# Kernel tuning notes

Measured on AMD Instinct MI355X. Metric: run time of the kernel, lower is better.

The kernel has to match this reference:

```python
import jax, jax.numpy as jnp
import numpy as np


def _gather_nbrs(atoms, edges):
    # atoms [B,N,F], edges [B,N,D] (neighbor indices) -> [B,N,D,F]
    return jax.vmap(lambda a, e: a[e])(atoms, edges)


def _linear(x, W, b):
    return x @ W + b


def setup_inputs() -> dict:
    key = jax.random.key(0)
    ks = jax.random.split(key, 32)
    B, Nm, Dm, Fa, Fb = 64, 64, 6, 37, 6      # molecules
    Np, Dp, Fp = 512, 12, 480                  # proteins
    HM, HP, NC = 128, 128, 1

    def rn(k, shape):
        return jax.random.normal(k, shape, jnp.float32) * 0.05

    return {
        'm_atoms': jax.random.normal(ks[0], (B, Nm, Fa), jnp.float32),
        'm_bonds': jax.random.normal(ks[1], (B, Nm, Dm, Fb), jnp.float32),
        'm_edges': jax.random.randint(ks[2], (B, Nm, Dm), 0, Nm, jnp.int32),
        'p_atoms': jax.random.normal(ks[3], (B, Np, Fp), jnp.float32),
        'p_edges': jax.random.randint(ks[4], (B, Np, Dp), 0, Np, jnp.int32),
        # GraphConv mol 1: in 43 = 37 atom + 6 bond
        'W1': rn(ks[5], (43, 128)), 'b1': jnp.zeros((128,), jnp.float32),
        # GraphConv mol 2: in 134 = 128 + 6
        'W2': rn(ks[6], (134, 128)), 'b2': jnp.zeros((128,), jnp.float32),
        # GraphConv_p 1/2
        'Wp1': rn(ks[7], (480, 200)), 'bp1': jnp.zeros((200,), jnp.float32),
        'Wp2': rn(ks[8], (200, 100)), 'bp2': jnp.zeros((100,), jnp.float32),
        # GraphOutput (134 -> hid_dim_m), GraphOutput_p (100 -> hid_dim_p)
        'Wo': rn(ks[9], (134, HM)), 'bo': jnp.zeros((HM,), jnp.float32),
        'Wop': rn(ks[10], (100, HP)), 'bop': jnp.zeros((HP,), jnp.float32),
        # FC stack
        'Wf1': rn(ks[11], (HM + HP, 100)), 'bf1': jnp.zeros((100,), jnp.float32),
        'Wf2': rn(ks[12], (100, 100)), 'bf2': jnp.zeros((100,), jnp.float32),
        'Wout': rn(ks[13], (100, NC)), 'bout': jnp.zeros((NC,), jnp.float32),
    }


def reference(m_atoms, m_bonds, m_edges, p_atoms, p_edges,
              W1, b1, W2, b2, Wp1, bp1, Wp2, bp2,
              Wo, bo, Wop, bop, Wf1, bf1, Wf2, bf2, Wout, bout):
    def gconv_mol(atoms, W, b):
        # self + summed-neighbor atom features, concat summed bond features
        nbr_sum = _gather_nbrs(atoms, m_edges).sum(2)           # [B,N,F]
        summed = jnp.concatenate([atoms + nbr_sum, m_bonds.sum(2)], axis=-1)
        return _linear(summed, W, b)

    def gconv_pro(atoms, W, b):
        nbr_sum = _gather_nbrs(atoms, p_edges).sum(2)
        return _linear(atoms + nbr_sum, W, b)

    a = jax.nn.relu(gconv_mol(m_atoms, W1, b1))
    a = jax.nn.relu(gconv_mol(a, W2, b2))
    # GraphOutput: tanh(linear(cat[atoms, bond_sum])) summed over atoms
    fp_m = jnp.tanh(_linear(jnp.concatenate([a, m_bonds.sum(2)], -1), Wo, bo)).sum(1)

    p = jax.nn.relu(gconv_pro(p_atoms, Wp1, bp1))
    p = jax.nn.relu(gconv_pro(p, Wp2, bp2))
    fp_p = jnp.tanh(_linear(p, Wop, bop)).sum(1)

    fp = jnp.concatenate([fp_m, fp_p], axis=1)
    # NOTE: source applies FC1 then FC2 with no activation in between
    fp = _linear(_linear(fp, Wf1, bf1), Wf2, bf2)
    return jax.nn.sigmoid(_linear(fp, Wout, bout))
```

## Files before the change

### kernel.cpp

```cpp
#include <hip/hip_runtime.h>
#include <cmath>

#define B   64
#define NM  64
#define DM  6
#define FA  37
#define FB  6
#define NP  512
#define DP  12
#define FPD 480
#define HM  128
#define HP  128

typedef _Float16 half8 __attribute__((ext_vector_type(8)));
typedef float f32x4 __attribute__((ext_vector_type(4)));

static const size_t OFF_FPP  = 0;
static const size_t OFF_Z    = OFF_FPP + (size_t)B*128;
static const size_t OFF_P    = OFF_Z   + (size_t)B*NP*200;
static const size_t OFF_W16  = OFF_P   + (size_t)B*NP*200 + 256;
#define W16_WT1   0
#define W16_WT2   107520
#define W16_WTOP  132608
#define W16_MW1T  148992
#define W16_MW2T  157184
#define W16_MWOT  177664
#define W16_TOT   198144

__device__ __forceinline__ float4 f4add(float4 a, float4 b) {
    return make_float4(a.x + b.x, a.y + b.y, a.z + b.z, a.w + b.w);
}

__device__ __forceinline__ half8 load_a_frag(const float* p) {
    float4 f0 = *(const float4*)(p);
    float4 f1 = *(const float4*)(p + 4);
    half8 h;
    h[0] = (_Float16)f0.x; h[1] = (_Float16)f0.y; h[2] = (_Float16)f0.z; h[3] = (_Float16)f0.w;
    h[4] = (_Float16)f1.x; h[5] = (_Float16)f1.y; h[6] = (_Float16)f1.z; h[7] = (_Float16)f1.w;
    return h;
}

__global__ void k_prep(const float* __restrict__ Wp1, const float* __restrict__ Wp2,
                       const float* __restrict__ Wop,
                       const float* __restrict__ W1,  const float* __restrict__ W2,
                       const float* __restrict__ Wo,  _Float16* __restrict__ w16) {
    int idx = blockIdx.x * 256 + threadIdx.x;
    if (idx < 224 * 480) {
        int n = idx / 480, k = idx % 480;
        w16[idx] = (n < 200) ? (_Float16)Wp1[k * 200 + n] : (_Float16)0.f;
    } else if (idx < W16_WTOP) {
        int r = idx - W16_WT2;
        int n = r / 224, k = r % 224;
        w16[idx] = (n < 100 && k < 200) ? (_Float16)Wp2[k * 100 + n] : (_Float16)0.f;
    } else if (idx < W16_MW1T) {
        int r = idx - W16_WTOP;
        int n = r >> 7, k = r & 127;
        w16[idx] = (k < 100) ? (_Float16)Wop[k * 128 + n] : (_Float16)0.f;
    } else if (idx < W16_MW2T) {
        int r = idx - W16_MW1T;
        int n = r >> 6, k = r & 63;
        w16[idx] = (k < 43) ? (_Float16)W1[k * 128 + n] : (_Float16)0.f;
    } else if (idx < W16_MWOT) {
        int r = idx - W16_MW2T;
        int n = r / 160, k = r % 160;
        w16[idx] = (k < 134) ? (_Float16)W2[k * 128 + n] : (_Float16)0.f;
    } else if (idx < W16_TOT) {
        int r = idx - W16_MWOT;
        int n = r / 160, k = r % 160;
        w16[idx] = (k < 134) ? (_Float16)Wo[k * 128 + n] : (_Float16)0.f;
    }
}

__global__ __launch_bounds__(256) void k_zp1(
        const float* __restrict__ A, const _Float16* __restrict__ Wt,
        float* __restrict__ Z) {
    int tid = threadIdx.x, lane = tid & 63, wid = tid >> 6;
    int rw = wid & 1, cw = wid >> 1;
    int rbase = blockIdx.x * 64 + rw * 32;
    int cbase = cw * 112;
    int lr = lane & 15, lk = (lane >> 4) * 8;
    f32x4 acc[2][7] = {};
    const float* Ar0 = A + (size_t)(rbase + lr) * FPD + lk;
    const float* Ar1 = A + (size_t)(rbase + 16 + lr) * FPD + lk;
    for (int k0 = 0; k0 < FPD; k0 += 32) {
        half8 a0 = load_a_frag(Ar0 + k0);
        half8 a1 = load_a_frag(Ar1 + k0);
        #pragma unroll
        for (int nt = 0; nt < 7; ++nt) {
            half8 b = *(const half8*)&Wt[(size_t)(cbase + nt * 16 + lr) * FPD + k0 + lk];
            acc[0][nt] = __builtin_amdgcn_mfma_f32_16x16x32_f16(a0, b, acc[0][nt], 0, 0, 0);
            acc[1][nt] = __builtin_amdgcn_mfma_f32_16x16x32_f16(a1, b, acc[1][nt], 0, 0, 0);
        }
    }
    int rj = (lane >> 4) * 4;
    #pragma unroll
    for (int nt = 0; nt < 7; ++nt) {
        int col = cbase + nt * 16 + lr;
        if (col < 200) {
            #pragma unroll
            for (int mt = 0; mt < 2; ++mt)
                #pragma unroll
                for (int j = 0; j < 4; ++j)
                    Z[(size_t)(rbase + mt * 16 + rj + j) * 200 + col] = acc[mt][nt][j];
        }
    }
}

__global__ __launch_bounds__(256) void k_ga1(
        const float* __restrict__ Z, const int* __restrict__ edges,
        const float* __restrict__ bias, float* __restrict__ out) {
    int bid = blockIdx.x;
    int x = bid & 7, j = bid >> 3;
    int b = (j >> 5) * 8 + x, tile = j & 31;
    int n0 = tile * 16, tid = threadIdx.x;
    __shared__ int e[16 * DP];
    if (tid < 16 * DP)
        e[tid] = edges[(b * NP + n0 + tid / DP) * DP + tid % DP];
    __syncthreads();
    const float4* Zb = (const float4*)(Z + (size_t)b * NP * 200);
    float4* ob = (float4*)(out + (size_t)b * NP * 200);
    const float4* b4 = (const float4*)bias;
    for (int idx = tid; idx < 16 * 50; idx += 256) {
        int r = idx / 50, c = idx % 50;
        float4 v = Zb[(n0 + r) * 50 + c];
        #pragma unroll
        for (int d = 0; d < DP; ++d) v = f4add(v, Zb[e[r * DP + d] * 50 + c]);
        v = f4add(v, b4[c]);
        ob[(n0 + r) * 50 + c] = make_float4(fmaxf(v.x, 0.f), fmaxf(v.y, 0.f),
                                            fmaxf(v.z, 0.f), fmaxf(v.w, 0.f));
    }
}

__global__ __launch_bounds__(256) void k_zp2(
        const float* __restrict__ A, const _Float16* __restrict__ Wt,
        float* __restrict__ Z) {
    int tid = threadIdx.x, lane = tid & 63, wid = tid >> 6;
    int rbase = blockIdx.x * 128 + wid * 32;
    int lr = lane & 15, lk = (lane >> 4) * 8;
    f32x4 acc[2][7] = {};
    const float* Ar0 = A + (size_t)(rbase + lr) * 200 + lk;
    const float* Ar1 = A + (size_t)(rbase + 16 + lr) * 200 + lk;
    for (int k0 = 0; k0 < 224; k0 += 32) {
        half8 a0 = load_a_frag(Ar0 + k0);
        half8 a1 = load_a_frag(Ar1 + k0);
        #pragma unroll
        for (int nt = 0; nt < 7; ++nt) {
            half8 b = *(const half8*)&Wt[(size_t)(nt * 16 + lr) * 224 + k0 + lk];
            acc[0][nt] = __builtin_amdgcn_mfma_f32_16x16x32_f16(a0, b, acc[0][nt], 0, 0, 0);
            acc[1][nt] = __builtin_amdgcn_mfma_f32_16x16x32_f16(a1, b, acc[1][nt], 0, 0, 0);
        }
    }
    int rj = (lane >> 4) * 4;
    #pragma unroll
    for (int nt = 0; nt < 7; ++nt) {
        int col = nt * 16 + lr;
        if (col < 100) {
            #pragma unroll
            for (int mt = 0; mt < 2; ++mt)
                #pragma unroll
                for (int j = 0; j < 4; ++j)
                    Z[(size_t)(rbase + mt * 16 + rj + j) * 100 + col] = acc[mt][nt][j];
        }
    }
}

__global__ __launch_bounds__(256) void k_ga2(
        const float* __restrict__ Z, const int* __restrict__ edges,
        const float* __restrict__ bias, float* __restrict__ out) {
    int bid = blockIdx.x;
    int x = bid & 7, j = bid >> 3;
    int b = (j >> 5) * 8 + x, tile = j & 31;
    int n0 = tile * 16, tid = threadIdx.x;
    __shared__ int e[16 * DP];
    if (tid < 16 * DP)
        e[tid] = edges[(b * NP + n0 + tid / DP) * DP + tid % DP];
    __syncthreads();
    const float4* Zb = (const float4*)(Z + (size_t)b * NP * 100);
    float4* ob = (float4*)(out + (size_t)b * NP * 100);
    const float4* b4 = (const float4*)bias;
    for (int idx = tid; idx < 16 * 25; idx += 256) {
        int r = idx / 25, c = idx % 25;
        float4 v = Zb[(n0 + r) * 25 + c];
        #pragma unroll
        for (int d = 0; d < DP; ++d) v = f4add(v, Zb[e[r * DP + d] * 25 + c]);
        v = f4add(v, b4[c]);
        ob[(n0 + r) * 25 + c] = make_float4(fmaxf(v.x, 0.f), fmaxf(v.y, 0.f),
                                            fmaxf(v.z, 0.f), fmaxf(v.w, 0.f));
    }
}

__global__ __launch_bounds__(256) void k_pout(
        const float* __restrict__ A, const _Float16* __restrict__ Wt,
        const float* __restrict__ bias, float* __restrict__ fpp) {
    int tid = threadIdx.x, lane = tid & 63, wid = tid >> 6;
    int rbase = blockIdx.x * 128 + wid * 32;
    int lr = lane & 15, lk = (lane >> 4) * 8;
    f32x4 acc[2][8] = {};
    const float* Ar0 = A + (size_t)(rbase + lr) * 100 + lk;
    const float* Ar1 = A + (size_t)(rbase + 16 + lr) * 100 + lk;
    for (int k0 = 0; k0 < 128; k0 += 32) {
        half8 a0 = load_a_frag(Ar0 + k0);
        half8 a1 = load_a_frag(Ar1 + k0);
        #pragma unroll
        for (int nt = 0; nt < 8; ++nt) {
            half8 b = *(const half8*)&Wt[(size_t)(nt * 16 + lr) * 128 + k0 + lk];
            acc[0][nt] = __builtin_amdgcn_mfma_f32_16x16x32_f16(a0, b, acc[0][nt], 0, 0, 0);
            acc[1][nt] = __builtin_amdgcn_mfma_f32_16x16x32_f16(a1, b, acc[1][nt], 0, 0, 0);
        }
    }
    int bmol = blockIdx.x >> 2;
    #pragma unroll
    for (int nt = 0; nt < 8; ++nt) {
        float bb = bias[nt * 16 + lr];
        float s = 0.f;
        #pragma unroll
        for (int mt = 0; mt < 2; ++mt)
            #pragma unroll
            for (int j = 0; j < 4; ++j)
                s += tanhf(acc[mt][nt][j] + bb);
        s += __shfl_xor(s, 16);
        s += __shfl_xor(s, 32);
        if (lane < 16) atomicAdd(&fpp[bmol * 128 + nt * 16 + lane], s);
    }
}

#define P_ATOM 40
#define P_S1   72
#define P_A    136
#define P_S23  168
__global__ __launch_bounds__(512) void k_mol(
        const float* __restrict__ m_atoms, const float* __restrict__ m_bonds,
        const int* __restrict__ m_edges,
        const _Float16* __restrict__ W1t, const _Float16* __restrict__ W2t,
        const _Float16* __restrict__ Wot,
        const float* __restrict__ b1, const float* __restrict__ b2,
        const float* __restrict__ bo,
        const float* __restrict__ fpp,
        const float* __restrict__ Wf1, const float* __restrict__ bf1,
        const float* __restrict__ Wf2, const float* __restrict__ bf2,
        const float* __restrict__ Wout, const float* __restrict__ bout,
        float* __restrict__ out) {
    int b = blockIdx.x, tid = threadIdx.x;
    __shared__ __align__(16) float smem[11464];
    float*     atoms_sh = smem;
    _Float16*  a1  = (_Float16*)smem;
    _Float16*  S1  = (_Float16*)(smem + 4352);
    _Float16*  S23 = (_Float16*)(smem + 4352);
    float*     bond  = smem + 9728;
    int*       edg   = (int*)(smem + 10112);
    float*     red   = smem + 10496;
    float*     fcb   = smem + 11008;

    const float* ga = m_atoms + (size_t)b * NM * FA;
    for (int i = tid; i < NM * FA; i += 512)
        atoms_sh[(i / FA) * P_ATOM + (i % FA)] = ga[i];
    if (tid < NM * DM) edg[tid] = m_edges[b * NM * DM + tid];
    if (tid < NM * FB) {
        int r = tid / FB, j = tid % FB;
        float s = 0.f;
        #pragma unroll
        for (int d = 0; d < DM; ++d) s += m_bonds[((size_t)(b * NM + r) * DM + d) * FB + j];
        bond[tid] = s;
    }
    __syncthreads();

    for (int i = tid; i < 64 * 64; i += 512) {
        int r = i >> 6, k = i & 63;
        float v = 0.f;
        if (k < FA) {
            v = atoms_sh[r * P_ATOM + k];
            #pragma unroll
            for (int d = 0; d < DM; ++d) v += atoms_sh[edg[r * DM + d] * P_ATOM + k];
        } else if (k < FA + FB) {
            v = bond[r * FB + (k - FA)];
        }
        S1[r * P_S1 + k] = (_Float16)v;
    }
    __syncthreads();

    int lane = tid & 63, wid = tid >> 6;
    int rw = wid & 3, cw = wid >> 2;
    int rbase = rw * 16, cbase = cw * 64;
    int lr = lane & 15, lkb = (lane >> 4) * 8, rj = (lane >> 4) * 4;

    {
        f32x4 acc[4] = {};
        for (int k0 = 0; k0 < 64; k0 += 32) {
            half8 a = *(const half8*)&S1[(rbase + lr) * P_S1 + k0 + lkb];
            #pragma unroll
            for (int nt = 0; nt < 4; ++nt) {
                half8 bf = *(const half8*)&W1t[(cbase + nt * 16 + lr) * 64 + k0 + lkb];
                acc[nt] = __builtin_amdgcn_mfma_f32_16x16x32_f16(a, bf, acc[nt], 0, 0, 0);
            }
        }
        #pragma unroll
        for (int nt = 0; nt < 4; ++nt) {
            int col = cbase + nt * 16 + lr;
            float bb = b1[col];
            #pragma unroll
            for (int j = 0; j < 4; ++j)
                a1[(rbase + rj + j) * P_A + col] = (_Float16)fmaxf(acc[nt][j] + bb, 0.f);
        }
    }
    __syncthreads();

    for (int i = tid; i < 64 * 160; i += 512) {
        int r = i / 160, k = i % 160;
        float v = 0.f;
        if (k < 128) {
            v = (float)a1[r * P_A + k];
            #pragma unroll
            for (int d = 0; d < DM; ++d) v += (float)a1[edg[r * DM + d] * P_A + k];
        } else if (k < 134) {
            v = bond[r * FB + (k - 128)];
        }
        S23[r * P_S23 + k] = (_Float16)v;
    }
    __syncthreads();

    f32x4 acc2[4] = {};
    for (int k0 = 0; k0 < 160; k0 += 32) {
        half8 a = *(const half8*)&S23[(rbase + lr) * P_S23 + k0 + lkb];
        #pragma unroll
        for (int nt = 0; nt < 4; ++nt) {
            half8 bf = *(const half8*)&W2t[(cbase + nt * 16 + lr) * 160 + k0 + lkb];
            acc2[nt] = __builtin_amdgcn_mfma_f32_16x16x32_f16(a, bf, acc2[nt], 0, 0, 0);
        }
    }
    __syncthreads();

    #pragma unroll
    for (int nt = 0; nt < 4; ++nt) {
        int col = cbase + nt * 16 + lr;
        float bb = b2[col];
        #pragma unroll
        for (int j = 0; j < 4; ++j)
            S23[(rbase + rj + j) * P_S23 + col] = (_Float16)fmaxf(acc2[nt][j] + bb, 0.f);
    }
    for (int i = tid; i < 64 * 32; i += 512) {
        int r = i >> 5, k = 128 + (i & 31);
        S23[r * P_S23 + k] = (k < 134) ? (_Float16)bond[r * FB + (k - 128)] : (_Float16)0.f;
    }
    __syncthreads();

    {
        f32x4 acc3[4] = {};
        for (int k0 = 0; k0 < 160; k0 += 32) {
            half8 a = *(const half8*)&S23[(rbase + lr) * P_S23 + k0 + lkb];
            #pragma unroll
            for (int nt = 0; nt < 4; ++nt) {
                half8 bf = *(const half8*)&Wot[(cbase + nt * 16 + lr) * 160 + k0 + lkb];
                acc3[nt] = __builtin_amdgcn_mfma_f32_16x16x32_f16(a, bf, acc3[nt], 0, 0, 0);
            }
        }
        #pragma unroll
        for (int nt = 0; nt < 4; ++nt) {
            int col = cbase + nt * 16 + lr;
            float bb = bo[col];
            float s = 0.f;
            #pragma unroll
            for (int j = 0; j < 4; ++j) s += tanhf(acc3[nt][j] + bb);
            s += __shfl_xor(s, 16);
            s += __shfl_xor(s, 32);
            if (lane < 16) red[rw * 128 + col] = s;
        }
    }
    __syncthreads();

    if (tid < 128)       fcb[tid] = red[tid] + red[128 + tid] + red[256 + tid] + red[384 + tid];
    else if (tid < 256)  fcb[tid] = fpp[b * 128 + (tid - 128)];
    __syncthreads();
    if (tid < 100) {
        float acc = bf1[tid];
        for (int k = 0; k < 256; ++k) acc = fmaf(fcb[k], Wf1[k * 100 + tid], acc);
        fcb[256 + tid] = acc;
    }
    __syncthreads();
    if (tid < 100) {
        float acc = bf2[tid];
        for (int k = 0; k < 100; ++k) acc = fmaf(fcb[256 + k], Wf2[k * 100 + tid], acc);
        fcb[356 + tid] = acc;
    }
    __syncthreads();
    if (tid < 64) {
        float v = fcb[356 + tid] * Wout[tid];
        if (tid + 64 < 100) v += fcb[356 + tid + 64] * Wout[tid + 64];
        #pragma unroll
        for (int off = 32; off > 0; off >>= 1) v += __shfl_down(v, off);
        if (tid == 0) out[b] = 1.f / (1.f + expf(-(v + bout[0])));
    }
}

extern "C" void kernel_launch(void* const* d_in, const int* in_sizes, int n_in,
                              void* d_out, int out_size, void* d_ws, size_t ws_size,
                              hipStream_t stream) {
    const float* m_atoms = (const float*)d_in[0];
    const float* m_bonds = (const float*)d_in[1];
    const int*   m_edges = (const int*)  d_in[2];
    const float* p_atoms = (const float*)d_in[3];
    const int*   p_edges = (const int*)  d_in[4];
    const float* W1   = (const float*)d_in[5];  const float* b1   = (const float*)d_in[6];
    const float* W2   = (const float*)d_in[7];  const float* b2   = (const float*)d_in[8];
    const float* Wp1  = (const float*)d_in[9];  const float* bp1  = (const float*)d_in[10];
    const float* Wp2  = (const float*)d_in[11]; const float* bp2  = (const float*)d_in[12];
    const float* Wo   = (const float*)d_in[13]; const float* bo   = (const float*)d_in[14];
    const float* Wop  = (const float*)d_in[15]; const float* bop  = (const float*)d_in[16];
    const float* Wf1  = (const float*)d_in[17]; const float* bf1  = (const float*)d_in[18];
    const float* Wf2  = (const float*)d_in[19]; const float* bf2  = (const float*)d_in[20];
    const float* Wout = (const float*)d_in[21]; const float* bout = (const float*)d_in[22];

    float* ws   = (float*)d_ws;
    float* fpp  = ws + OFF_FPP;
    float* zbuf = ws + OFF_Z;
    float* pbuf = ws + OFF_P;
    _Float16* w16 = (_Float16*)(ws + OFF_W16);

    hipMemsetAsync(fpp, 0, (size_t)B * 128 * sizeof(float), stream);
    k_prep<<<dim3((W16_TOT + 255) / 256), 256, 0, stream>>>(Wp1, Wp2, Wop, W1, W2, Wo, w16);

    k_zp1 <<<dim3(B * NP / 64), 256, 0, stream>>>(p_atoms, w16 + W16_WT1, zbuf);
    k_ga1 <<<dim3(B * NP / 16), 256, 0, stream>>>(zbuf, p_edges, bp1, pbuf);
    k_zp2 <<<dim3(B * NP / 128), 256, 0, stream>>>(pbuf, w16 + W16_WT2, zbuf);
    k_ga2 <<<dim3(B * NP / 16), 256, 0, stream>>>(zbuf, p_edges, bp2, pbuf);
    k_pout<<<dim3(B * NP / 128), 256, 0, stream>>>(pbuf, w16 + W16_WTOP, bop, fpp);

    k_mol <<<dim3(B), 512, 0, stream>>>(m_atoms, m_bonds, m_edges,
                                        w16 + W16_MW1T, w16 + W16_MW2T, w16 + W16_MWOT,
                                        b1, b2, bo, fpp,
                                        Wf1, bf1, Wf2, bf2, Wout, bout, (float*)d_out);
}
```

Before: 272.9 us.

## Fuse protein gather-aggregate into following GEMMs with fp16 intermediates

Removes the separate gather/aggregate kernels for both protein graph-conv layers. Each neighbor sum plus bias and ReLU is now computed directly as the MFMA A-fragment inside the next GEMM, so five protein kernels become three. The intermediate Z buffers are stored as fp16 with padded strides, roughly halving their traffic, and the biases are pre-converted to fp16. In exchange, neighbor sums accumulate in fp16, which adds rounding error and overflow risk. The zp1 tile is also halved to 16 rows per wave.

```diff
diff --git a/kernel.cpp b/kernel.cpp
--- a/kernel.cpp
+++ b/kernel.cpp
@@ -15,21 +15,19 @@
 typedef _Float16 half8 __attribute__((ext_vector_type(8)));
 typedef float f32x4 __attribute__((ext_vector_type(4)));
 
-static const size_t OFF_FPP  = 0;
-static const size_t OFF_Z    = OFF_FPP + (size_t)B*128;
-static const size_t OFF_P    = OFF_Z   + (size_t)B*NP*200;
-static const size_t OFF_W16  = OFF_P   + (size_t)B*NP*200 + 256;
+static const size_t OFF_FPP = 0;
+static const size_t OFF_Z1  = OFF_FPP + (size_t)B*128;
+static const size_t OFF_Z2  = OFF_Z1  + (size_t)32768*224/2;
+static const size_t OFF_W16 = OFF_Z2  + (size_t)32768*128/2;
 #define W16_WT1   0
 #define W16_WT2   107520
-#define W16_WTOP  132608
-#define W16_MW1T  148992
-#define W16_MW2T  157184
-#define W16_MWOT  177664
-#define W16_TOT   198144
-
-__device__ __forceinline__ float4 f4add(float4 a, float4 b) {
-    return make_float4(a.x + b.x, a.y + b.y, a.z + b.z, a.w + b.w);
-}
+#define W16_WTOP  136192
+#define W16_MW1T  152576
+#define W16_MW2T  160768
+#define W16_MWOT  181248
+#define W16_BP1   201728
+#define W16_BP2   201952
+#define W16_TOT   202080
 
 __device__ __forceinline__ half8 load_a_frag(const float* p) {
     float4 f0 = *(const float4*)(p);
@@ -43,9 +41,11 @@
 __global__ void k_prep(const float* __restrict__ Wp1, const float* __restrict__ Wp2,
                        const float* __restrict__ Wop,
                        const float* __restrict__ W1,  const float* __restrict__ W2,
-                       const float* __restrict__ Wo,  _Float16* __restrict__ w16) {
+                       const float* __restrict__ Wo,
+                       const float* __restrict__ bp1, const float* __restrict__ bp2,
+                       _Float16* __restrict__ w16) {
     int idx = blockIdx.x * 256 + threadIdx.x;
-    if (idx < 224 * 480) {
+    if (idx < W16_WT2) {
         int n = idx / 480, k = idx % 480;
         w16[idx] = (n < 200) ? (_Float16)Wp1[k * 200 + n] : (_Float16)0.f;
     } else if (idx < W16_WTOP) {
@@ -64,163 +64,133 @@
         int r = idx - W16_MW2T;
         int n = r / 160, k = r % 160;
         w16[idx] = (k < 134) ? (_Float16)W2[k * 128 + n] : (_Float16)0.f;
-    } else if (idx < W16_TOT) {
+    } else if (idx < W16_BP1) {
         int r = idx - W16_MWOT;
         int n = r / 160, k = r % 160;
         w16[idx] = (k < 134) ? (_Float16)Wo[k * 128 + n] : (_Float16)0.f;
+    } else if (idx < W16_BP2) {
+        int k = idx - W16_BP1;
+        w16[idx] = (k < 200) ? (_Float16)bp1[k] : (_Float16)0.f;
+    } else if (idx < W16_TOT) {
+        int k = idx - W16_BP2;
+        w16[idx] = (k < 100) ? (_Float16)bp2[k] : (_Float16)0.f;
     }
 }
 
 __global__ __launch_bounds__(256) void k_zp1(
         const float* __restrict__ A, const _Float16* __restrict__ Wt,
-        float* __restrict__ Z) {
+        _Float16* __restrict__ Z) {
     int tid = threadIdx.x, lane = tid & 63, wid = tid >> 6;
     int rw = wid & 1, cw = wid >> 1;
-    int rbase = blockIdx.x * 64 + rw * 32;
+    int rbase = blockIdx.x * 32 + rw * 16;
     int cbase = cw * 112;
-    int lr = lane & 15, lk = (lane >> 4) * 8;
-    f32x4 acc[2][7] = {};
-    const float* Ar0 = A + (size_t)(rbase + lr) * FPD + lk;
-    const float* Ar1 = A + (size_t)(rbase + 16 + lr) * FPD + lk;
+    int lr = lane & 15, q = lane >> 4, lkb = q * 8;
+    f32x4 acc[7] = {};
+    const float* Ar = A + (size_t)(rbase + lr) * FPD + lkb;
     for (int k0 = 0; k0 < FPD; k0 += 32) {
-        half8 a0 = load_a_frag(Ar0 + k0);
-        half8 a1 = load_a_frag(Ar1 + k0);
+        half8 a = load_a_frag(Ar + k0);
         #pragma unroll
         for (int nt = 0; nt < 7; ++nt) {
-            half8 b = *(const half8*)&Wt[(size_t)(cbase + nt * 16 + lr) * FPD + k0 + lk];
-            acc[0][nt] = __builtin_amdgcn_mfma_f32_16x16x32_f16(a0, b, acc[0][nt], 0, 0, 0);
-            acc[1][nt] = __builtin_amdgcn_mfma_f32_16x16x32_f16(a1, b, acc[1][nt], 0, 0, 0);
-        }
-    }
-    int rj = (lane >> 4) * 4;
+            half8 b = *(const half8*)&Wt[(size_t)(cbase + nt * 16 + lr) * FPD + k0 + lkb];
+            acc[nt] = __builtin_amdgcn_mfma_f32_16x16x32_f16(a, b, acc[nt], 0, 0, 0);
+        }
+    }
+    int rj = q * 4;
     #pragma unroll
     for (int nt = 0; nt < 7; ++nt) {
         int col = cbase + nt * 16 + lr;
-        if (col < 200) {
-            #pragma unroll
-            for (int mt = 0; mt < 2; ++mt)
-                #pragma unroll
-                for (int j = 0; j < 4; ++j)
-                    Z[(size_t)(rbase + mt * 16 + rj + j) * 200 + col] = acc[mt][nt][j];
-        }
-    }
-}
-
-__global__ __launch_bounds__(256) void k_ga1(
-        const float* __restrict__ Z, const int* __restrict__ edges,
-        const float* __restrict__ bias, float* __restrict__ out) {
+        #pragma unroll
+        for (int j = 0; j < 4; ++j)
+            Z[(size_t)(rbase + rj + j) * 224 + col] = (_Float16)acc[nt][j];
+    }
+}
+
+__global__ __launch_bounds__(256) void k_zp2f(
+        const _Float16* __restrict__ Z1, const int* __restrict__ edges,
+        const _Float16* __restrict__ bp1h, const _Float16* __restrict__ Wt,
+        _Float16* __restrict__ Z2) {
     int bid = blockIdx.x;
-    int x = bid & 7, j = bid >> 3;
-    int b = (j >> 5) * 8 + x, tile = j & 31;
-    int n0 = tile * 16, tid = threadIdx.x;
-    __shared__ int e[16 * DP];
-    if (tid < 16 * DP)
-        e[tid] = edges[(b * NP + n0 + tid / DP) * DP + tid % DP];
-    __syncthreads();
-    const float4* Zb = (const float4*)(Z + (size_t)b * NP * 200);
-    float4* ob = (float4*)(out + (size_t)b * NP * 200);
-    const float4* b4 = (const float4*)bias;
-    for (int idx = tid; idx < 16 * 50; idx += 256) {
-        int r = idx / 50, c = idx % 50;
-        float4 v = Zb[(n0 + r) * 50 + c];
-        #pragma unroll
-        for (int d = 0; d < DP; ++d) v = f4add(v, Zb[e[r * DP + d] * 50 + c]);
-        v = f4add(v, b4[c]);
-        ob[(n0 + r) * 50 + c] = make_float4(fmaxf(v.x, 0.f), fmaxf(v.y, 0.f),
-                                            fmaxf(v.z, 0.f), fmaxf(v.w, 0.f));
-    }
-}
-
-__global__ __launch_bounds__(256) void k_zp2(
-        const float* __restrict__ A, const _Float16* __restrict__ Wt,
-        float* __restrict__ Z) {
+    int t = (bid & 7) * 64 + (bid >> 3);
     int tid = threadIdx.x, lane = tid & 63, wid = tid >> 6;
-    int rbase = blockIdx.x * 128 + wid * 32;
-    int lr = lane & 15, lk = (lane >> 4) * 8;
-    f32x4 acc[2][7] = {};
-    const float* Ar0 = A + (size_t)(rbase + lr) * 200 + lk;
-    const float* Ar1 = A + (size_t)(rbase + 16 + lr) * 200 + lk;
+    int lr = lane & 15, q = lane >> 4, lkb = q * 8;
+    int rbase = t * 64 + wid * 16;
+    int gr = rbase + lr;
+    int mb = gr >> 9, lrow = gr & 511;
+    const int* ep = edges + (size_t)gr * DP;
+    const _Float16* zb = Z1 + ((size_t)mb << 9) * 224;
+    const _Float16* src[13];
+    src[0] = zb + (size_t)lrow * 224;
+    #pragma unroll
+    for (int d = 0; d < 12; ++d) src[d + 1] = zb + (size_t)ep[d] * 224;
+
+    f32x4 acc[7] = {};
     for (int k0 = 0; k0 < 224; k0 += 32) {
-        half8 a0 = load_a_frag(Ar0 + k0);
-        half8 a1 = load_a_frag(Ar1 + k0);
+        int ko = k0 + lkb;
+        half8 s = *(const half8*)(src[0] + ko);
+        #pragma unroll
+        for (int d = 1; d < 13; ++d) s = s + *(const half8*)(src[d] + ko);
+        s = s + *(const half8*)(bp1h + ko);
+        #pragma unroll
+        for (int j = 0; j < 8; ++j) if (s[j] < (_Float16)0.f) s[j] = (_Float16)0.f;
         #pragma unroll
         for (int nt = 0; nt < 7; ++nt) {
-            half8 b = *(const half8*)&Wt[(size_t)(nt * 16 + lr) * 224 + k0 + lk];
-            acc[0][nt] = __builtin_amdgcn_mfma_f32_16x16x32_f16(a0, b, acc[0][nt], 0, 0, 0);
-            acc[1][nt] = __builtin_amdgcn_mfma_f32_16x16x32_f16(a1, b, acc[1][nt], 0, 0, 0);
-        }
-    }
-    int rj = (lane >> 4) * 4;
+            half8 b = *(const half8*)&Wt[(size_t)(nt * 16 + lr) * 224 + ko];
+            acc[nt] = __builtin_amdgcn_mfma_f32_16x16x32_f16(s, b, acc[nt], 0, 0, 0);
+        }
+    }
+    int rj = q * 4;
     #pragma unroll
     for (int nt = 0; nt < 7; ++nt) {
         int col = nt * 16 + lr;
-        if (col < 100) {
-            #pragma unroll
-            for (int mt = 0; mt < 2; ++mt)
-                #pragma unroll
-                for (int j = 0; j < 4; ++j)
-                    Z[(size_t)(rbase + mt * 16 + rj + j) * 100 + col] = acc[mt][nt][j];
-        }
-    }
-}
-
-__global__ __launch_bounds__(256) void k_ga2(
-        const float* __restrict__ Z, const int* __restrict__ edges,
-        const float* __restrict__ bias, float* __restrict__ out) {
+        #pragma unroll
+        for (int j = 0; j < 4; ++j)
+            Z2[(size_t)(rbase + rj + j) * 128 + col] = (_Float16)acc[nt][j];
+    }
+}
+
+__global__ __launch_bounds__(256) void k_pof(
+        const _Float16* __restrict__ Z2, const int* __restrict__ edges,
+        const _Float16* __restrict__ bp2h, const _Float16* __restrict__ Wt,
+        const float* __restrict__ bop, float* __restrict__ fpp) {
     int bid = blockIdx.x;
-    int x = bid & 7, j = bid >> 3;
-    int b = (j >> 5) * 8 + x, tile = j & 31;
-    int n0 = tile * 16, tid = threadIdx.x;
-    __shared__ int e[16 * DP];
-    if (tid < 16 * DP)
-        e[tid] = edges[(b * NP + n0 + tid / DP) * DP + tid % DP];
-    __syncthreads();
-    const float4* Zb = (const float4*)(Z + (size_t)b * NP * 100);
-    float4* ob = (float4*)(out + (size_t)b * NP * 100);
-    const float4* b4 = (const float4*)bias;
-    for (int idx = tid; idx < 16 * 25; idx += 256) {
-        int r = idx / 25, c = idx % 25;
-        float4 v = Zb[(n0 + r) * 25 + c];
-        #pragma unroll
-        for (int d = 0; d < DP; ++d) v = f4add(v, Zb[e[r * DP + d] * 25 + c]);
-        v = f4add(v, b4[c]);
-        ob[(n0 + r) * 25 + c] = make_float4(fmaxf(v.x, 0.f), fmaxf(v.y, 0.f),
-                                            fmaxf(v.z, 0.f), fmaxf(v.w, 0.f));
-    }
-}
-
-__global__ __launch_bounds__(256) void k_pout(
-        const float* __restrict__ A, const _Float16* __restrict__ Wt,
-        const float* __restrict__ bias, float* __restrict__ fpp) {
+    int t = (bid & 7) * 64 + (bid >> 3);
     int tid = threadIdx.x, lane = tid & 63, wid = tid >> 6;
-    int rbase = blockIdx.x * 128 + wid * 32;
-    int lr = lane & 15, lk = (lane >> 4) * 8;
-    f32x4 acc[2][8] = {};
-    const float* Ar0 = A + (size_t)(rbase + lr) * 100 + lk;
-    const float* Ar1 = A + (size_t)(rbase + 16 + lr) * 100 + lk;
+    int lr = lane & 15, q = lane >> 4, lkb = q * 8;
+    int rbase = t * 64 + wid * 16;
+    int gr = rbase + lr;
+    int mb = gr >> 9, lrow = gr & 511;
+    const int* ep = edges + (size_t)gr * DP;
+    const _Float16* zb = Z2 + ((size_t)mb << 9) * 128;
+    const _Float16* src[13];
+    src[0] = zb + (size_t)lrow * 128;
+    #pragma unroll
+    for (int d = 0; d < 12; ++d) src[d + 1] = zb + (size_t)ep[d] * 128;
+
+    f32x4 acc[8] = {};
     for (int k0 = 0; k0 < 128; k0 += 32) {
-        half8 a0 = load_a_frag(Ar0 + k0);
-        half8 a1 = load_a_frag(Ar1 + k0);
+        int ko = k0 + lkb;
+        half8 s = *(const half8*)(src[0] + ko);
+        #pragma unroll
+        for (int d = 1; d < 13; ++d) s = s + *(const half8*)(src[d] + ko);
+        s = s + *(const half8*)(bp2h + ko);
+        #pragma unroll
+        for (int j = 0; j < 8; ++j) if (s[j] < (_Float16)0.f) s[j] = (_Float16)0.f;
         #pragma unroll
         for (int nt = 0; nt < 8; ++nt) {
-            half8 b = *(const half8*)&Wt[(size_t)(nt * 16 + lr) * 128 + k0 + lk];
-            acc[0][nt] = __builtin_amdgcn_mfma_f32_16x16x32_f16(a0, b, acc[0][nt], 0, 0, 0);
-            acc[1][nt] = __builtin_amdgcn_mfma_f32_16x16x32_f16(a1, b, acc[1][nt], 0, 0, 0);
-        }
-    }
-    int bmol = blockIdx.x >> 2;
+            half8 b = *(const half8*)&Wt[(size_t)(nt * 16 + lr) * 128 + ko];
+            acc[nt] = __builtin_amdgcn_mfma_f32_16x16x32_f16(s, b, acc[nt], 0, 0, 0);
+        }
+    }
     #pragma unroll
     for (int nt = 0; nt < 8; ++nt) {
-        float bb = bias[nt * 16 + lr];
+        int col = nt * 16 + lr;
+        float bb = bop[col];
         float s = 0.f;
         #pragma unroll
-        for (int mt = 0; mt < 2; ++mt)
-            #pragma unroll
-            for (int j = 0; j < 4; ++j)
-                s += tanhf(acc[mt][nt][j] + bb);
+        for (int j = 0; j < 4; ++j) s += tanhf(acc[nt][j] + bb);
         s += __shfl_xor(s, 16);
         s += __shfl_xor(s, 32);
-        if (lane < 16) atomicAdd(&fpp[bmol * 128 + nt * 16 + lane], s);
+        if (lane < 16) atomicAdd(&fpp[mb * 128 + col], s);
     }
 }
 
@@ -411,18 +381,19 @@
 
     float* ws   = (float*)d_ws;
     float* fpp  = ws + OFF_FPP;
-    float* zbuf = ws + OFF_Z;
-    float* pbuf = ws + OFF_P;
+    _Float16* z1  = (_Float16*)(ws + OFF_Z1);
+    _Float16* z2  = (_Float16*)(ws + OFF_Z2);
     _Float16* w16 = (_Float16*)(ws + OFF_W16);
 
     hipMemsetAsync(fpp, 0, (size_t)B * 128 * sizeof(float), stream);
-    k_prep<<<dim3((W16_TOT + 255) / 256), 256, 0, stream>>>(Wp1, Wp2, Wop, W1, W2, Wo, w16);
-
-    k_zp1 <<<dim3(B * NP / 64), 256, 0, stream>>>(p_atoms, w16 + W16_WT1, zbuf);
-    k_ga1 <<<dim3(B * NP / 16), 256, 0, stream>>>(zbuf, p_edges, bp1, pbuf);
-    k_zp2 <<<dim3(B * NP / 128), 256, 0, stream>>>(pbuf, w16 + W16_WT2, zbuf);
-    k_ga2 <<<dim3(B * NP / 16), 256, 0, stream>>>(zbuf, p_edges, bp2, pbuf);
-    k_pout<<<dim3(B * NP / 128), 256, 0, stream>>>(pbuf, w16 + W16_WTOP, bop, fpp);
+    k_prep<<<dim3((W16_TOT + 255) / 256), 256, 0, stream>>>(
+        Wp1, Wp2, Wop, W1, W2, Wo, bp1, bp2, w16);
+
+    k_zp1 <<<dim3(B * NP / 32), 256, 0, stream>>>(p_atoms, w16 + W16_WT1, z1);
+    k_zp2f<<<dim3(B * NP / 64), 256, 0, stream>>>(z1, p_edges, w16 + W16_BP1,
+                                                  w16 + W16_WT2, z2);
+    k_pof <<<dim3(B * NP / 64), 256, 0, stream>>>(z2, p_edges, w16 + W16_BP2,
+                                                  w16 + W16_WTOP, bop, fpp);
 
     k_mol <<<dim3(B), 512, 0, stream>>>(m_atoms, m_bonds, m_edges,
                                         w16 + W16_MW1T, w16 + W16_MW2T, w16 + W16_MWOT,
```

Result: faster. 260.7 us (-4.5%).
